# Optimization experiments

Hardware: AMD Instinct MI355X
Metric: run time of the kernel (lower is better)

## Reference

```python
import jax, jax.numpy as jnp
import numpy as np

N_NODES = 100000
N_EDGES = 300000
N_TYPES = 3
HID = 128
EMB = 64
N_GRAPHS = 4096
T_STEPS = 4


def setup_inputs() -> dict:
    key = jax.random.key(0)
    ks = jax.random.split(key, 12)
    s = 1.0 / np.sqrt(HID)
    return {
        "node_features": jax.random.normal(ks[0], (N_NODES, HID), jnp.float32),
        "edge_index": jax.random.randint(ks[1], (N_TYPES, 2, N_EDGES), 0, N_NODES),
        "node_to_graph_id": jnp.sort(jax.random.randint(ks[2], (N_NODES,), 0, N_GRAPHS)),
        "W_msg": jax.random.normal(ks[3], (N_TYPES, HID, HID), jnp.float32) * s,
        "b_msg": jnp.zeros((N_TYPES, HID), jnp.float32),
        "W_ih": jax.random.normal(ks[4], (3 * HID, HID), jnp.float32) * s,
        "W_hh": jax.random.normal(ks[5], (3 * HID, HID), jnp.float32) * s,
        "b_ih": jnp.zeros((3 * HID,), jnp.float32),
        "b_hh": jnp.zeros((3 * HID,), jnp.float32),
        "W_proj": jax.random.normal(ks[6], (EMB, HID), jnp.float32) * s,
        "b_proj": jnp.zeros((EMB,), jnp.float32),
        "W_gate": jax.random.normal(ks[7], (EMB, HID), jnp.float32) * s,
        "b_gate": jnp.zeros((EMB,), jnp.float32),
    }


def _gru_cell(m, h, W_ih, W_hh, b_ih, b_hh):
    # torch.nn.GRUCell math; gates ordered (r, z, n)
    gi = m @ W_ih.T + b_ih          # [N, 3H]
    gh = h @ W_hh.T + b_hh          # [N, 3H]
    i_r, i_z, i_n = jnp.split(gi, 3, axis=-1)
    h_r, h_z, h_n = jnp.split(gh, 3, axis=-1)
    r = jax.nn.sigmoid(i_r + h_r)
    z = jax.nn.sigmoid(i_z + h_z)
    n = jnp.tanh(i_n + r * h_n)
    return (1.0 - z) * n + z * h


def reference(node_features, edge_index, node_to_graph_id,
              W_msg, b_msg, W_ih, W_hh, b_ih, b_hh,
              W_proj, b_proj, W_gate, b_gate):
    h = node_features  # [N, H]

    def per_type(eidx, W, b, h):
        src, dst = eidx[0], eidx[1]
        m = h[src] @ W + b  # gather + per-edge-type linear, [E, H]
        return jax.ops.segment_sum(m, dst, num_segments=N_NODES)

    for _ in range(T_STEPS):  # fixed small T: python loop is fine
        msgs = jax.vmap(per_type, in_axes=(0, 0, 0, None))(edge_index, W_msg, b_msg, h)
        m = msgs.sum(axis=0)  # [N, H] aggregated over edge types
        h = _gru_cell(m, h, W_ih, W_hh, b_ih, b_hh)

    # gated index_add graph readout (mlp_down is identity)
    proj = h @ W_proj.T + b_proj                 # [N, E]
    gate = jax.nn.sigmoid(h @ W_gate.T + b_gate)  # [N, E]
    graph_feats = jax.ops.segment_sum(gate * proj, node_to_graph_id,
                                      num_segments=N_GRAPHS)
    return graph_feats
```

## Files before the change

### kernel.cpp

```cpp
#include <hip/hip_runtime.h>
#include <hip/hip_bf16.h>
#include <math.h>

#define NN 100000
#define NNP 100096
#define NE 300000
#define HID 128
#define EMB 64
#define NG 4096
#define DEG_CAP 32
#define XS 512

typedef __bf16 bf16x8 __attribute__((ext_vector_type(8)));
typedef float  f32x16 __attribute__((ext_vector_type(16)));
typedef short  short8 __attribute__((ext_vector_type(8)));

typedef const __attribute__((address_space(1))) unsigned int* gas_u32;
typedef __attribute__((address_space(3))) unsigned int* las_u32;

__device__ __forceinline__ void gload16(const void* g, void* l) {
    __builtin_amdgcn_global_load_lds((gas_u32)g, (las_u32)l, 16, 0, 0);
}

__device__ __forceinline__ float bf2f(unsigned short u) {
    unsigned int x = ((unsigned int)u) << 16;
    return __builtin_bit_cast(float, x);
}
__device__ __forceinline__ unsigned short f2bf(float f) {
    unsigned int x = __builtin_bit_cast(unsigned int, f);
    unsigned int r = x + 0x7fff + ((x >> 16) & 1);
    return (unsigned short)(r >> 16);
}
__device__ __forceinline__ float sigm(float x) { return 1.f / (1.f + __expf(-x)); }

__global__ __launch_bounds__(256) void k_init(const float* __restrict__ nf,
                                              unsigned short* __restrict__ Y,
                                              unsigned short* __restrict__ X) {
    int id = blockIdx.x * 256 + threadIdx.x;
    int n = id >> 7, c = id & 127;
    unsigned short hv = (n < NN) ? f2bf(nf[(long)n * HID + c]) : (unsigned short)0;
    Y[(long)n * HID + c] = hv;
    X[(long)n * XS + 384 + c] = hv;
}

__global__ __launch_bounds__(256) void k_build_csr(const int* __restrict__ ei,
                                                   int* __restrict__ deg,
                                                   int* __restrict__ csr) {
    int id = blockIdx.x * 256 + threadIdx.x;
    if (id >= 3 * NE) return;
    int t = id / NE;
    int i = id - t * NE;
    int src = ei[(t * 2 + 0) * NE + i];
    int dst = ei[(t * 2 + 1) * NE + i];
    int p = atomicAdd(&deg[t * NN + dst], 1);
    if (p < DEG_CAP) csr[((long)t * NN + dst) * DEG_CAP + p] = src;
}

__global__ __launch_bounds__(256) void k_pack_deg(const int* __restrict__ deg,
                                                  int4* __restrict__ degp) {
    int n = blockIdx.x * 256 + threadIdx.x;
    if (n >= NNP) return;
    int4 v; v.x = 0; v.y = 0; v.z = 0; v.w = 0;
    if (n < NN) { v.x = deg[n]; v.y = deg[NN + n]; v.z = deg[2 * NN + n]; }
    degp[n] = v;
}

__global__ __launch_bounds__(512) void k_build_w(const float* __restrict__ Wmsg,
                                                 const float* __restrict__ Wih,
                                                 const float* __restrict__ Whh,
                                                 unsigned short* __restrict__ Bf) {
    int np = blockIdx.x;
    int k = threadIdx.x;
    int c = np >> 2, sec = np & 3;
    float v = 0.f;
    if (k < 384) {
        if (sec < 3) {
            int t = k >> 7, kk = k & 127;
            const float* wm = Wmsg + ((long)t * HID + kk) * HID;
            const float* wi = Wih + (long)(sec * HID + c) * HID;
            float s = 0.f;
            for (int j = 0; j < HID; j++) s += wm[j] * wi[j];
            v = s;
        }
    } else {
        int kk = k - 384;
        if (sec == 0)      v = Whh[(long)c * HID + kk];
        else if (sec == 1) v = Whh[(long)(HID + c) * HID + kk];
        else if (sec == 3) v = Whh[(long)(2 * HID + c) * HID + kk];
    }
    int nb = np >> 5, nl = np & 31;
    int k16 = k >> 4, kgg = (k >> 3) & 1, e = k & 7;
    Bf[((((nb * 32 + k16) * 2 + kgg) * 32 + nl) << 3) + e] = f2bf(v);
}

__global__ __launch_bounds__(512) void k_build_bias(const float* __restrict__ bih,
                                                    const float* __restrict__ bhh,
                                                    const float* __restrict__ bmsg,
                                                    const float* __restrict__ Wih,
                                                    float* __restrict__ bbig,
                                                    float* __restrict__ Bdeg) {
    int np = threadIdx.x;
    int c = np >> 2, sec = np & 3;
    float b;
    if (sec == 0)      b = bih[c] + bhh[c];
    else if (sec == 1) b = bih[HID + c] + bhh[HID + c];
    else if (sec == 2) b = bih[2 * HID + c];
    else               b = bhh[2 * HID + c];
    bbig[np] = b;
    for (int t = 0; t < 3; t++) {
        float s = 0.f;
        if (sec < 3) {
            const float* wi = Wih + (long)(sec * HID + c) * HID;
            const float* bm = bmsg + t * HID;
            for (int j = 0; j < HID; j++) s += bm[j] * wi[j];
        }
        Bdeg[t * 512 + np] = s;
    }
}

__global__ __launch_bounds__(256) void k_agg(const unsigned short* __restrict__ Y,
                                             unsigned short* __restrict__ X,
                                             const int* __restrict__ deg,
                                             const int* __restrict__ csr) {
    const int lane = threadIdx.x & 63;
    const long n = (long)blockIdx.x * 4 + (threadIdx.x >> 6);
    const int g = lane >> 4;
    const int c16 = lane & 15;
    const int l31 = lane & 31;

    int d[3], il[3];
#pragma unroll
    for (int t = 0; t < 3; t++) {
        int dt = deg[t * NN + n];
        d[t] = dt > DEG_CAP ? DEG_CAP : dt;
        il[t] = csr[((long)t * NN + n) * DEG_CAP + l31];
    }
#pragma unroll
    for (int t = 0; t < 3; t++) {
        float acc[8] = {0.f, 0.f, 0.f, 0.f, 0.f, 0.f, 0.f, 0.f};
        int rounds = (d[t] + 3) >> 2;
        for (int r = 0; r < rounds; r++) {
            int j = r * 4 + g;
            int idx = __shfl(il[t], j & 31);
            if (j < d[t]) {
                short8 v = *(const short8*)(Y + (long)idx * HID + c16 * 8);
#pragma unroll
                for (int q = 0; q < 8; q++) acc[q] += bf2f((unsigned short)v[q]);
            }
        }
#pragma unroll
        for (int q = 0; q < 8; q++) {
            acc[q] += __shfl_xor(acc[q], 16);
            acc[q] += __shfl_xor(acc[q], 32);
        }
        if (g == 0) {
            short8 o;
#pragma unroll
            for (int q = 0; q < 8; q++) o[q] = (short)f2bf(acc[q]);
            *(short8*)(X + n * XS + t * HID + c16 * 8) = o;
        }
    }
}

__global__ __launch_bounds__(512, 4) void k_gru_mfma(
        const unsigned short* __restrict__ X,
        unsigned short* __restrict__ Xh,
        const unsigned short* __restrict__ Y,
        unsigned short* __restrict__ Yw,
        const unsigned short* __restrict__ Bf,
        const float* __restrict__ bbig, const float* __restrict__ Bdeg,
        const int4* __restrict__ degp) {
    __shared__ char lds[32768];

    const int tid = threadIdx.x;
    const int lane = tid & 63;
    const int wv = tid >> 6;
    const int r31 = lane & 31;
    const int kg = lane >> 5;
    const long row0 = (long)blockIdx.x * 64;

    f32x16 acc[2][2];
#pragma unroll
    for (int i = 0; i < 2; i++)
#pragma unroll
        for (int j = 0; j < 2; j++) acc[i][j] = (f32x16)(0.0f);

    const char* pAl = (const char*)X + (row0 + r31) * 1024 + kg * 16;
#define STAGE_A(HALF)                                                           \
    {                                                                           \
        _Pragma("unroll")                                                       \
        for (int jj = 0; jj < 4; jj++) {                                        \
            const int f = wv * 4 + jj;                                          \
            gload16(pAl + (f & 1) * 32768 + ((HALF) * 16 + (f >> 1)) * 32,      \
                    lds + f * 1024);                                            \
        }                                                                       \
    }

    const unsigned short* pB0 = Bf + (wv * 2 + 0) * 16384 + lane * 8;
    const unsigned short* pB1 = Bf + (wv * 2 + 1) * 16384 + lane * 8;

    STAGE_A(0);
    __syncthreads();

#pragma unroll
    for (int k16l = 0; k16l < 16; k16l++) {
        short8 a0 = *(const short8*)(lds + (k16l * 2 + 0) * 1024 + lane * 16);
        short8 a1 = *(const short8*)(lds + (k16l * 2 + 1) * 1024 + lane * 16);
        short8 b0 = *(const short8*)(pB0 + k16l * 512);
        short8 b1 = *(const short8*)(pB1 + k16l * 512);
        acc[0][0] = __builtin_amdgcn_mfma_f32_32x32x16_bf16(
            __builtin_bit_cast(bf16x8, a0), __builtin_bit_cast(bf16x8, b0), acc[0][0], 0, 0, 0);
        acc[0][1] = __builtin_amdgcn_mfma_f32_32x32x16_bf16(
            __builtin_bit_cast(bf16x8, a0), __builtin_bit_cast(bf16x8, b1), acc[0][1], 0, 0, 0);
        acc[1][0] = __builtin_amdgcn_mfma_f32_32x32x16_bf16(
            __builtin_bit_cast(bf16x8, a1), __builtin_bit_cast(bf16x8, b0), acc[1][0], 0, 0, 0);
        acc[1][1] = __builtin_amdgcn_mfma_f32_32x32x16_bf16(
            __builtin_bit_cast(bf16x8, a1), __builtin_bit_cast(bf16x8, b1), acc[1][1], 0, 0, 0);
    }

    __syncthreads();
    STAGE_A(1);
    __syncthreads();

#pragma unroll
    for (int k16l = 0; k16l < 16; k16l++) {
        const int k16g = 16 + k16l;
        short8 a0 = *(const short8*)(lds + (k16l * 2 + 0) * 1024 + lane * 16);
        short8 a1 = *(const short8*)(lds + (k16l * 2 + 1) * 1024 + lane * 16);
        short8 b0 = *(const short8*)(pB0 + k16g * 512);
        short8 b1 = *(const short8*)(pB1 + k16g * 512);
        acc[0][0] = __builtin_amdgcn_mfma_f32_32x32x16_bf16(
            __builtin_bit_cast(bf16x8, a0), __builtin_bit_cast(bf16x8, b0), acc[0][0], 0, 0, 0);
        acc[0][1] = __builtin_amdgcn_mfma_f32_32x32x16_bf16(
            __builtin_bit_cast(bf16x8, a0), __builtin_bit_cast(bf16x8, b1), acc[0][1], 0, 0, 0);
        acc[1][0] = __builtin_amdgcn_mfma_f32_32x32x16_bf16(
            __builtin_bit_cast(bf16x8, a1), __builtin_bit_cast(bf16x8, b0), acc[1][0], 0, 0, 0);
        acc[1][1] = __builtin_amdgcn_mfma_f32_32x32x16_bf16(
            __builtin_bit_cast(bf16x8, a1), __builtin_bit_cast(bf16x8, b1), acc[1][1], 0, 0, 0);
    }

    float* EX = (float*)lds;
    const int ch = tid & 127;
    const int rbase = tid >> 7;
    const float4 bb = *(const float4*)(bbig + ch * 4);
    const float4 e0 = *(const float4*)(Bdeg + ch * 4);
    const float4 e1 = *(const float4*)(Bdeg + 512 + ch * 4);
    const float4 e2 = *(const float4*)(Bdeg + 1024 + ch * 4);

#pragma unroll
    for (int b = 0; b < 4; b++) {
        __syncthreads();
        {
            const int mt = b >> 1;
            const int qh = (b & 1) * 8;
#pragma unroll
            for (int ct = 0; ct < 2; ct++) {
                int col = wv * 64 + ct * 32 + r31;
#pragma unroll
                for (int qq = 0; qq < 8; qq++) {
                    int rwl = (qq & 3) + 8 * (qq >> 2) + 4 * kg;
                    EX[rwl * 512 + col] = acc[mt][ct][qh + qq];
                }
            }
        }
        __syncthreads();
#pragma unroll
        for (int i = 0; i < 4; i++) {
            int rwl = rbase + 4 * i;
            long grow = row0 + b * 16 + rwl;
            int4 dg = degp[grow];
            float dgx = (float)dg.x, dgy = (float)dg.y, dgz = (float)dg.z;
            float4 v = *(const float4*)(EX + rwl * 512 + ch * 4);
            float Sr = v.x + bb.x + dgx * e0.x + dgy * e1.x + dgz * e2.x;
            float Sz = v.y + bb.y + dgx * e0.y + dgy * e1.y + dgz * e2.y;
            float In = v.z + bb.z + dgx * e0.z + dgy * e1.z + dgz * e2.z;
            float Hn = v.w + bb.w;
            float rr = sigm(Sr);
            float zz = sigm(Sz);
            float tt = In + rr * Hn;
            float ee = __expf(2.f * tt);
            float nn = 1.f - 2.f / (ee + 1.f);
            float hv = (1.f - zz) * nn + zz * bf2f(Y[grow * HID + ch]);
            unsigned short hb = f2bf(hv);
            Yw[grow * HID + ch] = hb;
            Xh[grow * XS + 384 + ch] = hb;
        }
    }
}

__global__ __launch_bounds__(256) void k_readout(const unsigned short* __restrict__ Y,
                                                 const int* __restrict__ n2g,
                                                 const float* __restrict__ Wp,
                                                 const float* __restrict__ bp,
                                                 const float* __restrict__ Wg,
                                                 const float* __restrict__ bg,
                                                 float* __restrict__ out) {
    __shared__ float hs[32][132];
    __shared__ float Ws[64][129];
    int tid = threadIdx.x;
    long row0 = (long)blockIdx.x * 32;
    int rg = tid >> 5, cg = tid & 31;
    float acc[4][4];
#pragma unroll
    for (int r = 0; r < 4; r++)
#pragma unroll
        for (int c = 0; c < 4; c++) acc[r][c] = 0.f;

#pragma unroll
    for (int p = 0; p < 2; p++) {
        int e = p * 256 + tid;
        int r = e >> 4, c8 = e & 15;
        short8 v = *(const short8*)(Y + (row0 + r) * HID + c8 * 8);
#pragma unroll
        for (int j = 0; j < 8; j++) hs[r][c8 * 8 + j] = bf2f((unsigned short)v[j]);
    }
    for (int kc = 0; kc < 128; kc += 64) {
        __syncthreads();
#pragma unroll
        for (int p = 0; p < 8; p++) {
            int idx = p * 256 + tid;
            int j = idx >> 4, q = idx & 15;
            const float* Wsrc = (j < 64) ? Wp : Wg;
            float4 w = *(const float4*)&Wsrc[(j & 63) * HID + kc + q * 4];
            Ws[q * 4 + 0][j] = w.x;
            Ws[q * 4 + 1][j] = w.y;
            Ws[q * 4 + 2][j] = w.z;
            Ws[q * 4 + 3][j] = w.w;
        }
        __syncthreads();
#pragma unroll 8
        for (int k = 0; k < 64; k++) {
            float a[4], w[4];
#pragma unroll
            for (int r = 0; r < 4; r++) a[r] = hs[rg * 4 + r][kc + k];
#pragma unroll
            for (int c = 0; c < 4; c++) w[c] = Ws[k][cg + 32 * c];
#pragma unroll
            for (int r = 0; r < 4; r++)
#pragma unroll
                for (int c = 0; c < 4; c++) acc[r][c] += a[r] * w[c];
        }
    }
#pragma unroll
    for (int r = 0; r < 4; r++) {
        long row = row0 + rg * 4 + r;
        if (row < NN) {
            int g = n2g[row];
            float pv0 = acc[r][0] + bp[cg];
            float pv1 = acc[r][1] + bp[cg + 32];
            float gv0 = acc[r][2] + bg[cg];
            float gv1 = acc[r][3] + bg[cg + 32];
            atomicAdd(&out[g * EMB + cg],      pv0 * sigm(gv0));
            atomicAdd(&out[g * EMB + cg + 32], pv1 * sigm(gv1));
        }
    }
}

extern "C" void kernel_launch(void* const* d_in, const int* in_sizes, int n_in,
                              void* d_out, int out_size, void* d_ws, size_t ws_size,
                              hipStream_t stream) {
    const float* node_features = (const float*)d_in[0];
    const int*   edge_index    = (const int*)d_in[1];
    const int*   n2g           = (const int*)d_in[2];
    const float* W_msg         = (const float*)d_in[3];
    const float* b_msg         = (const float*)d_in[4];
    const float* W_ih          = (const float*)d_in[5];
    const float* W_hh          = (const float*)d_in[6];
    const float* b_ih          = (const float*)d_in[7];
    const float* b_hh          = (const float*)d_in[8];
    const float* W_proj        = (const float*)d_in[9];
    const float* b_proj        = (const float*)d_in[10];
    const float* W_gate        = (const float*)d_in[11];
    const float* b_gate        = (const float*)d_in[12];

    char* ws = (char*)d_ws;
    unsigned short* X    = (unsigned short*)(ws);
    unsigned short* Y    = (unsigned short*)(ws + 102498304);
    unsigned short* Bf   = (unsigned short*)(ws + 128122880);
    float*          bbig = (float*)         (ws + 128647168);
    float*          Bdeg = (float*)         (ws + 128649216);
    int4*           degp = (int4*)          (ws + 128655360);
    int*            deg  = (int*)           (ws + 130256896);
    int*            csr  = (int*)           (ws + 131456896);

    float* out = (float*)d_out;

    hipMemsetAsync(out, 0, (size_t)NG * EMB * sizeof(float), stream);
    hipMemsetAsync(deg, 0, (size_t)3 * NN * sizeof(int), stream);

    k_init<<<dim3((NNP * HID) / 256), dim3(256), 0, stream>>>(node_features, Y, X);
    k_build_csr<<<dim3((3 * NE + 255) / 256), dim3(256), 0, stream>>>(edge_index, deg, csr);
    k_pack_deg<<<dim3(NNP / 256), dim3(256), 0, stream>>>(deg, degp);
    k_build_w<<<dim3(512), dim3(512), 0, stream>>>(W_msg, W_ih, W_hh, Bf);
    k_build_bias<<<dim3(1), dim3(512), 0, stream>>>(b_ih, b_hh, b_msg, W_ih, bbig, Bdeg);

    for (int step = 0; step < 4; step++) {
        k_agg<<<dim3(NN / 4), dim3(256), 0, stream>>>(Y, X, deg, csr);
        k_gru_mfma<<<dim3(NNP / 64), dim3(512), 0, stream>>>(X, X, Y, Y, Bf,
                                                             bbig, Bdeg, degp);
    }
    k_readout<<<dim3(NN / 32), dim3(256), 0, stream>>>(Y, n2g, W_proj, b_proj,
                                                       W_gate, b_gate, out);
}
```

Baseline: 824.1 us.

## Split GRU GEMM over two column blocks and move hidden copy into aggregation

```diff
diff --git a/kernel.cpp b/kernel.cpp
--- a/kernel.cpp
+++ b/kernel.cpp
@@ -21,6 +21,9 @@
 __device__ __forceinline__ void gload16(const void* g, void* l) {
     __builtin_amdgcn_global_load_lds((gas_u32)g, (las_u32)l, 16, 0, 0);
 }
+__device__ __forceinline__ void gload16nt(const void* g, void* l) {
+    __builtin_amdgcn_global_load_lds((gas_u32)g, (las_u32)l, 16, 0, 2);
+}
 
 __device__ __forceinline__ float bf2f(unsigned short u) {
     unsigned int x = ((unsigned int)u) << 16;
@@ -34,13 +37,10 @@
 __device__ __forceinline__ float sigm(float x) { return 1.f / (1.f + __expf(-x)); }
 
 __global__ __launch_bounds__(256) void k_init(const float* __restrict__ nf,
-                                              unsigned short* __restrict__ Y,
-                                              unsigned short* __restrict__ X) {
+                                              unsigned short* __restrict__ Y) {
     int id = blockIdx.x * 256 + threadIdx.x;
     int n = id >> 7, c = id & 127;
-    unsigned short hv = (n < NN) ? f2bf(nf[(long)n * HID + c]) : (unsigned short)0;
-    Y[(long)n * HID + c] = hv;
-    X[(long)n * XS + 384 + c] = hv;
+    Y[(long)n * HID + c] = (n < NN) ? f2bf(nf[(long)n * HID + c]) : (unsigned short)0;
 }
 
 __global__ __launch_bounds__(256) void k_build_csr(const int* __restrict__ ei,
@@ -160,117 +160,100 @@
             *(short8*)(X + n * XS + t * HID + c16 * 8) = o;
         }
     }
+    if (g == 1) {
+        short8 v = *(const short8*)(Y + n * HID + c16 * 8);
+        *(short8*)(X + n * XS + 384 + c16 * 8) = v;
+    }
 }
 
 __global__ __launch_bounds__(512, 4) void k_gru_mfma(
         const unsigned short* __restrict__ X,
-        unsigned short* __restrict__ Xh,
         const unsigned short* __restrict__ Y,
         unsigned short* __restrict__ Yw,
         const unsigned short* __restrict__ Bf,
         const float* __restrict__ bbig, const float* __restrict__ Bdeg,
         const int4* __restrict__ degp) {
-    __shared__ char lds[32768];
+    __shared__ char lds[65536];
 
     const int tid = threadIdx.x;
     const int lane = tid & 63;
     const int wv = tid >> 6;
     const int r31 = lane & 31;
     const int kg = lane >> 5;
-    const long row0 = (long)blockIdx.x * 64;
-
-    f32x16 acc[2][2];
-#pragma unroll
-    for (int i = 0; i < 2; i++)
-#pragma unroll
-        for (int j = 0; j < 2; j++) acc[i][j] = (f32x16)(0.0f);
-
-    const char* pAl = (const char*)X + (row0 + r31) * 1024 + kg * 16;
-#define STAGE_A(HALF)                                                           \
-    {                                                                           \
-        _Pragma("unroll")                                                       \
-        for (int jj = 0; jj < 4; jj++) {                                        \
-            const int f = wv * 4 + jj;                                          \
-            gload16(pAl + (f & 1) * 32768 + ((HALF) * 16 + (f >> 1)) * 32,      \
-                    lds + f * 1024);                                            \
-        }                                                                       \
-    }
-
-    const unsigned short* pB0 = Bf + (wv * 2 + 0) * 16384 + lane * 8;
-    const unsigned short* pB1 = Bf + (wv * 2 + 1) * 16384 + lane * 8;
-
-    STAGE_A(0);
+    const int bnN = blockIdx.x;
+    const long row0 = (long)blockIdx.y * 64;
+
+    f32x16 acc0 = (f32x16)(0.0f);
+    f32x16 acc1 = (f32x16)(0.0f);
+
+    {
+        const char* base = (const char*)X + (row0 + r31) * 1024 + kg * 16;
+#pragma unroll
+        for (int jj = 0; jj < 8; jj++) {
+            const int f = wv * 8 + jj;
+            gload16nt(base + (f & 1) * 32768 + (f >> 1) * 32, lds + f * 1024);
+        }
+    }
+
+    const unsigned short* pB = Bf + (long)(bnN * 8 + wv) * 16384 + lane * 8;
+
+    short8 bs0 = *(const short8*)(pB);
+    short8 bs1 = *(const short8*)(pB + 512);
+    short8 bs2 = *(const short8*)(pB + 1024);
+    short8 bs3 = *(const short8*)(pB + 1536);
+
     __syncthreads();
 
 #pragma unroll
-    for (int k16l = 0; k16l < 16; k16l++) {
-        short8 a0 = *(const short8*)(lds + (k16l * 2 + 0) * 1024 + lane * 16);
-        short8 a1 = *(const short8*)(lds + (k16l * 2 + 1) * 1024 + lane * 16);
-        short8 b0 = *(const short8*)(pB0 + k16l * 512);
-        short8 b1 = *(const short8*)(pB1 + k16l * 512);
-        acc[0][0] = __builtin_amdgcn_mfma_f32_32x32x16_bf16(
-            __builtin_bit_cast(bf16x8, a0), __builtin_bit_cast(bf16x8, b0), acc[0][0], 0, 0, 0);
-        acc[0][1] = __builtin_amdgcn_mfma_f32_32x32x16_bf16(
-            __builtin_bit_cast(bf16x8, a0), __builtin_bit_cast(bf16x8, b1), acc[0][1], 0, 0, 0);
-        acc[1][0] = __builtin_amdgcn_mfma_f32_32x32x16_bf16(
-            __builtin_bit_cast(bf16x8, a1), __builtin_bit_cast(bf16x8, b0), acc[1][0], 0, 0, 0);
-        acc[1][1] = __builtin_amdgcn_mfma_f32_32x32x16_bf16(
-            __builtin_bit_cast(bf16x8, a1), __builtin_bit_cast(bf16x8, b1), acc[1][1], 0, 0, 0);
-    }
-
-    __syncthreads();
-    STAGE_A(1);
-    __syncthreads();
-
-#pragma unroll
-    for (int k16l = 0; k16l < 16; k16l++) {
-        const int k16g = 16 + k16l;
-        short8 a0 = *(const short8*)(lds + (k16l * 2 + 0) * 1024 + lane * 16);
-        short8 a1 = *(const short8*)(lds + (k16l * 2 + 1) * 1024 + lane * 16);
-        short8 b0 = *(const short8*)(pB0 + k16g * 512);
-        short8 b1 = *(const short8*)(pB1 + k16g * 512);
-        acc[0][0] = __builtin_amdgcn_mfma_f32_32x32x16_bf16(
-            __builtin_bit_cast(bf16x8, a0), __builtin_bit_cast(bf16x8, b0), acc[0][0], 0, 0, 0);
-        acc[0][1] = __builtin_amdgcn_mfma_f32_32x32x16_bf16(
-            __builtin_bit_cast(bf16x8, a0), __builtin_bit_cast(bf16x8, b1), acc[0][1], 0, 0, 0);
-        acc[1][0] = __builtin_amdgcn_mfma_f32_32x32x16_bf16(
-            __builtin_bit_cast(bf16x8, a1), __builtin_bit_cast(bf16x8, b0), acc[1][0], 0, 0, 0);
-        acc[1][1] = __builtin_amdgcn_mfma_f32_32x32x16_bf16(
-            __builtin_bit_cast(bf16x8, a1), __builtin_bit_cast(bf16x8, b1), acc[1][1], 0, 0, 0);
+    for (int it = 0; it < 32; it++) {
+        short8 a0 = *(const short8*)(lds + (it * 2 + 0) * 1024 + lane * 16);
+        short8 a1 = *(const short8*)(lds + (it * 2 + 1) * 1024 + lane * 16);
+        short8 b;
+        if ((it & 3) == 0) b = bs0;
+        else if ((it & 3) == 1) b = bs1;
+        else if ((it & 3) == 2) b = bs2;
+        else b = bs3;
+        if (it + 4 < 32) {
+            const short8 nb = *(const short8*)(pB + (it + 4) * 512);
+            if ((it & 3) == 0) bs0 = nb;
+            else if ((it & 3) == 1) bs1 = nb;
+            else if ((it & 3) == 2) bs2 = nb;
+            else bs3 = nb;
+        }
+        acc0 = __builtin_amdgcn_mfma_f32_32x32x16_bf16(
+            __builtin_bit_cast(bf16x8, a0), __builtin_bit_cast(bf16x8, b), acc0, 0, 0, 0);
+        acc1 = __builtin_amdgcn_mfma_f32_32x32x16_bf16(
+            __builtin_bit_cast(bf16x8, a1), __builtin_bit_cast(bf16x8, b), acc1, 0, 0, 0);
     }
 
     float* EX = (float*)lds;
-    const int ch = tid & 127;
-    const int rbase = tid >> 7;
-    const float4 bb = *(const float4*)(bbig + ch * 4);
-    const float4 e0 = *(const float4*)(Bdeg + ch * 4);
-    const float4 e1 = *(const float4*)(Bdeg + 512 + ch * 4);
-    const float4 e2 = *(const float4*)(Bdeg + 1024 + ch * 4);
+    const int ch = lane;
+    const int gch = bnN * 64 + ch;
+    const float4 bb = *(const float4*)(bbig + bnN * 256 + ch * 4);
+    const float4 e0 = *(const float4*)(Bdeg + bnN * 256 + ch * 4);
+    const float4 e1 = *(const float4*)(Bdeg + 512 + bnN * 256 + ch * 4);
+    const float4 e2 = *(const float4*)(Bdeg + 1024 + bnN * 256 + ch * 4);
 
 #pragma unroll
     for (int b = 0; b < 4; b++) {
         __syncthreads();
         {
-            const int mt = b >> 1;
             const int qh = (b & 1) * 8;
-#pragma unroll
-            for (int ct = 0; ct < 2; ct++) {
-                int col = wv * 64 + ct * 32 + r31;
-#pragma unroll
-                for (int qq = 0; qq < 8; qq++) {
-                    int rwl = (qq & 3) + 8 * (qq >> 2) + 4 * kg;
-                    EX[rwl * 512 + col] = acc[mt][ct][qh + qq];
-                }
+            const int col = wv * 32 + r31;
+#pragma unroll
+            for (int qq = 0; qq < 8; qq++) {
+                int rwl = (qq & 3) + 8 * (qq >> 2) + 4 * kg;
+                EX[rwl * 256 + col] = (b >> 1) ? acc1[qh + qq] : acc0[qh + qq];
             }
         }
         __syncthreads();
 #pragma unroll
-        for (int i = 0; i < 4; i++) {
-            int rwl = rbase + 4 * i;
+        for (int i = 0; i < 2; i++) {
+            int rwl = wv + 8 * i;
             long grow = row0 + b * 16 + rwl;
             int4 dg = degp[grow];
             float dgx = (float)dg.x, dgy = (float)dg.y, dgz = (float)dg.z;
-            float4 v = *(const float4*)(EX + rwl * 512 + ch * 4);
+            float4 v = *(const float4*)(EX + rwl * 256 + ch * 4);
             float Sr = v.x + bb.x + dgx * e0.x + dgy * e1.x + dgz * e2.x;
             float Sz = v.y + bb.y + dgx * e0.y + dgy * e1.y + dgz * e2.y;
             float In = v.z + bb.z + dgx * e0.z + dgy * e1.z + dgz * e2.z;
@@ -280,10 +263,8 @@
             float tt = In + rr * Hn;
             float ee = __expf(2.f * tt);
             float nn = 1.f - 2.f / (ee + 1.f);
-            float hv = (1.f - zz) * nn + zz * bf2f(Y[grow * HID + ch]);
-            unsigned short hb = f2bf(hv);
-            Yw[grow * HID + ch] = hb;
-            Xh[grow * XS + 384 + ch] = hb;
+            float hv = (1.f - zz) * nn + zz * bf2f(Y[grow * HID + gch]);
+            Yw[grow * HID + gch] = f2bf(hv);
         }
     }
 }
@@ -388,7 +369,7 @@
     hipMemsetAsync(out, 0, (size_t)NG * EMB * sizeof(float), stream);
     hipMemsetAsync(deg, 0, (size_t)3 * NN * sizeof(int), stream);
 
-    k_init<<<dim3((NNP * HID) / 256), dim3(256), 0, stream>>>(node_features, Y, X);
+    k_init<<<dim3((NNP * HID) / 256), dim3(256), 0, stream>>>(node_features, Y);
     k_build_csr<<<dim3((3 * NE + 255) / 256), dim3(256), 0, stream>>>(edge_index, deg, csr);
     k_pack_deg<<<dim3(NNP / 256), dim3(256), 0, stream>>>(deg, degp);
     k_build_w<<<dim3(512), dim3(512), 0, stream>>>(W_msg, W_ih, W_hh, Bf);
@@ -396,8 +377,8 @@
 
     for (int step = 0; step < 4; step++) {
         k_agg<<<dim3(NN / 4), dim3(256), 0, stream>>>(Y, X, deg, csr);
-        k_gru_mfma<<<dim3(NNP / 64), dim3(512), 0, stream>>>(X, X, Y, Y, Bf,
-                                                             bbig, Bdeg, degp);
+        k_gru_mfma<<<dim3(2, NNP / 64), dim3(512), 0, stream>>>(X, Y, Y, Bf,
+                                                                bbig, Bdeg, degp);
     }
     k_readout<<<dim3(NN / 32), dim3(256), 0, stream>>>(Y, n2g, W_proj, b_proj,
                                                        W_gate, b_gate, out);
```

Measured after the change: 972.7 us. 18.0% more time.
